# Kernel optimization log

Hardware: AMD Instinct MI355X
Metric: run time of the kernel (lower is better)

## Reference

```python
import jax, jax.numpy as jnp
import numpy as np

ALPHA = 0.2      # LeakyReLU negative slope
NEG = -9e15      # mask fill value from pyGAT dense layer
N, F, H = 4096, 512, 8
NH = F // H      # per-head hidden = 64


def setup_inputs() -> dict:
    key = jax.random.key(0)
    ks = jax.random.split(key, 8)
    x = jax.random.normal(ks[0], (N, F), jnp.float32)
    left = jnp.arange(N, dtype=jnp.int32)  # unused by forward (matches source)
    adj = (jax.random.uniform(ks[1], (N, N)) < 0.01).astype(jnp.float32)
    adj = jnp.minimum(adj + jnp.eye(N, dtype=jnp.float32), 1.0)  # self loops
    Ws = jax.random.normal(ks[2], (H, F, NH), jnp.float32) * (1.0 / np.sqrt(F))
    a1 = jax.random.normal(ks[3], (H, NH), jnp.float32) * 0.1
    a2 = jax.random.normal(ks[4], (H, NH), jnp.float32) * 0.1
    Wo = jax.random.normal(ks[5], (F, F), jnp.float32) * (1.0 / np.sqrt(F))
    ao1 = jax.random.normal(ks[6], (F,), jnp.float32) * 0.1
    ao2 = jax.random.normal(ks[7], (F,), jnp.float32) * 0.1
    return dict(x=x, left=left, adj=adj, Ws=Ws, a1=a1, a2=a2, Wo=Wo, ao1=ao1, ao2=ao2)


def _gat_layer(h, W, a_src, a_dst, adj, concat):
    # h: [N, Fin], W: [Fin, nh]
    Wh = h @ W                                   # [N, nh]
    e = (Wh @ a_src)[:, None] + (Wh @ a_dst)[None, :]   # [N, N]
    e = jnp.where(adj > 0, jax.nn.leaky_relu(e, ALPHA), NEG)
    att = jax.nn.softmax(e, axis=-1)             # row softmax over neighbors
    out = att @ Wh                               # [N, nh]
    return jax.nn.elu(out) if concat else out


def reference(x, left, adj, Ws, a1, a2, Wo, ao1, ao2):
    # multi-head attention (concat=True per head)
    heads = jax.vmap(lambda W, s, d: _gat_layer(x, W, s, d, adj, True))(Ws, a1, a2)  # [H, N, NH]
    hcat = jnp.transpose(heads, (1, 0, 2)).reshape(x.shape[0], H * NH)              # [N, F]
    # output attention layer (concat=False) followed by outer ELU
    out = _gat_layer(hcat, Wo, ao1, ao2, adj, False)
    return jax.nn.elu(out)
```

## Files before the change

kernel.cpp:

```cpp
#include <hip/hip_runtime.h>
#include <hip/hip_bf16.h>
#include <math.h>


#define GN 4096
#define GF 512

typedef __attribute__((ext_vector_type(8))) short bf16x8;
typedef __attribute__((ext_vector_type(4))) float f32x4;
typedef __attribute__((ext_vector_type(2))) _Float16 f16x2;

__device__ inline unsigned short f2bf(float f) {
    unsigned u = __float_as_uint(f);
    return (unsigned short)((u + 0x7fffu + ((u >> 16) & 1u)) >> 16);
}
__device__ inline float bf2f(unsigned short h) {
    return __uint_as_float((unsigned)h << 16);
}
__device__ inline void split2(float v, unsigned short& h, unsigned short& l) {
    h = f2bf(v);
    l = f2bf(v - bf2f(h));
}
__device__ inline void gl16(const void* g, void* l) {
    __builtin_amdgcn_global_load_lds((const __attribute__((address_space(1))) unsigned int*)g,
                                     (__attribute__((address_space(3))) unsigned int*)l, 16, 0, 0);
}

__global__ __launch_bounds__(256) void prep(
        const float* __restrict__ Ws, const float* __restrict__ Wo,
        const float* __restrict__ x,
        unsigned short* __restrict__ wshi, unsigned short* __restrict__ wslo,
        unsigned short* __restrict__ wohi, unsigned short* __restrict__ wolo,
        unsigned short* __restrict__ xhi, unsigned short* __restrict__ xlo) {
    __shared__ float T[64][65];
    int b = blockIdx.x;
    const int t = threadIdx.x;
    if (b < 64) {
        const int h = b >> 3, f0 = (b & 7) * 64;
        #pragma unroll
        for (int i = 0; i < 16; ++i) {
            int idx = i * 256 + t;
            int fr = idx >> 6, k = idx & 63;
            T[fr][k] = Ws[h * 32768 + (f0 + fr) * 64 + k];
        }
        __syncthreads();
        #pragma unroll
        for (int i = 0; i < 16; ++i) {
            int idx = i * 256 + t;
            int k = idx >> 6, fr = idx & 63;
            unsigned short hh, ll;
            split2(T[fr][k], hh, ll);
            size_t dst = (size_t)(h * 64 + k) * 512 + f0 + fr;
            wshi[dst] = hh; wslo[dst] = ll;
        }
        return;
    }
    b -= 64;
    if (b < 64) {
        const int c0 = (b >> 3) * 64, f0 = (b & 7) * 64;
        #pragma unroll
        for (int i = 0; i < 16; ++i) {
            int idx = i * 256 + t;
            int fr = idx >> 6, k = idx & 63;
            T[fr][k] = Wo[(size_t)(f0 + fr) * 512 + c0 + k];
        }
        __syncthreads();
        #pragma unroll
        for (int i = 0; i < 16; ++i) {
            int idx = i * 256 + t;
            int k = idx >> 6, fr = idx & 63;
            unsigned short hh, ll;
            split2(T[fr][k], hh, ll);
            size_t dst = (size_t)(c0 + k) * 512 + f0 + fr;
            wohi[dst] = hh; wolo[dst] = ll;
        }
        return;
    }
    b -= 64;
    {
        int i = b * 256 + t;
        float4 v = ((const float4*)x)[i];
        ushort4 h, l;
        split2(v.x, h.x, l.x); split2(v.y, h.y, l.y);
        split2(v.z, h.z, l.z); split2(v.w, h.w, l.w);
        ((ushort4*)xhi)[i] = h;
        ((ushort4*)xlo)[i] = l;
    }
}

__global__ __launch_bounds__(256) void gemm_3t(
        const unsigned short* __restrict__ Ahi, const unsigned short* __restrict__ Alo,
        const unsigned short* __restrict__ Bhi, const unsigned short* __restrict__ Blo,
        const float* __restrict__ a1v, const float* __restrict__ a2v,
        _Float16* __restrict__ C, float* __restrict__ sdst, float* __restrict__ ddst,
        int M, int K, int Nc) {
    __shared__ char lds[65536];
    const int t = threadIdx.x, lane = t & 63, wid = t >> 6;
    const int blk = blockIdx.x;
    const int bmI = (blk & 7) | ((blk >> 6) << 3);
    const int bnI = (blk >> 3) & 7;
    const int bm0 = bmI * 64, bn0 = bnI * 64;
    const int r0 = t >> 3;
    const int sc8 = (((t & 7) ^ ((t >> 3) & 7)) << 3);
    const size_t aoff = (size_t)(bm0 + r0) * K + sc8;
    const size_t boff = (size_t)(bn0 + r0) * K + sc8;
    const size_t half = (size_t)32 * K;

    auto stage = [&](char* dst, int k0) {
        gl16(Ahi + aoff + k0,        dst + 0 * 4096 + t * 16);
        gl16(Ahi + aoff + half + k0, dst + 1 * 4096 + t * 16);
        gl16(Alo + aoff + k0,        dst + 2 * 4096 + t * 16);
        gl16(Alo + aoff + half + k0, dst + 3 * 4096 + t * 16);
        gl16(Bhi + boff + k0,        dst + 4 * 4096 + t * 16);
        gl16(Bhi + boff + half + k0, dst + 5 * 4096 + t * 16);
        gl16(Blo + boff + k0,        dst + 6 * 4096 + t * 16);
        gl16(Blo + boff + half + k0, dst + 7 * 4096 + t * 16);
    };

    f32x4 acc00 = {0,0,0,0}, acc01 = {0,0,0,0}, acc10 = {0,0,0,0}, acc11 = {0,0,0,0};
    const int mq = (wid >> 1) * 32, nq = (wid & 1) * 32;
    const int rl = lane & 15, hl = lane >> 4;
    const int swz = rl & 7;

    auto compute = [&](const char* Lb) {
        const char* Ah_ = Lb;
        const char* Al_ = Lb + 8192;
        const char* Bh_ = Lb + 16384;
        const char* Bl_ = Lb + 24576;
        #pragma unroll
        for (int s = 0; s < 2; ++s) {
            const int ch = ((s * 4 + hl) ^ swz) * 16;
            const int ra0 = (mq + rl) * 128, ra1 = ra0 + 16 * 128;
            const int rb0 = (nq + rl) * 128, rb1 = rb0 + 16 * 128;
            bf16x8 A0h = *(const bf16x8*)(Ah_ + ra0 + ch);
            bf16x8 A1h = *(const bf16x8*)(Ah_ + ra1 + ch);
            bf16x8 A0l = *(const bf16x8*)(Al_ + ra0 + ch);
            bf16x8 A1l = *(const bf16x8*)(Al_ + ra1 + ch);
            bf16x8 B0h = *(const bf16x8*)(Bh_ + rb0 + ch);
            bf16x8 B1h = *(const bf16x8*)(Bh_ + rb1 + ch);
            bf16x8 B0l = *(const bf16x8*)(Bl_ + rb0 + ch);
            bf16x8 B1l = *(const bf16x8*)(Bl_ + rb1 + ch);
            acc00 = __builtin_amdgcn_mfma_f32_16x16x32_bf16(A0h, B0h, acc00, 0, 0, 0);
            acc01 = __builtin_amdgcn_mfma_f32_16x16x32_bf16(A0h, B1h, acc01, 0, 0, 0);
            acc10 = __builtin_amdgcn_mfma_f32_16x16x32_bf16(A1h, B0h, acc10, 0, 0, 0);
            acc11 = __builtin_amdgcn_mfma_f32_16x16x32_bf16(A1h, B1h, acc11, 0, 0, 0);
            acc00 = __builtin_amdgcn_mfma_f32_16x16x32_bf16(A0h, B0l, acc00, 0, 0, 0);
            acc01 = __builtin_amdgcn_mfma_f32_16x16x32_bf16(A0h, B1l, acc01, 0, 0, 0);
            acc10 = __builtin_amdgcn_mfma_f32_16x16x32_bf16(A1h, B0l, acc10, 0, 0, 0);
            acc11 = __builtin_amdgcn_mfma_f32_16x16x32_bf16(A1h, B1l, acc11, 0, 0, 0);
            acc00 = __builtin_amdgcn_mfma_f32_16x16x32_bf16(A0l, B0h, acc00, 0, 0, 0);
            acc01 = __builtin_amdgcn_mfma_f32_16x16x32_bf16(A0l, B1h, acc01, 0, 0, 0);
            acc10 = __builtin_amdgcn_mfma_f32_16x16x32_bf16(A1l, B0h, acc10, 0, 0, 0);
            acc11 = __builtin_amdgcn_mfma_f32_16x16x32_bf16(A1l, B1h, acc11, 0, 0, 0);
        }
    };

    stage(lds, 0);
    __syncthreads();
    const int NT = K / 64;
    for (int st = 0; st < NT; ++st) {
        char* cur = lds + (st & 1) * 32768;
        if (st + 1 < NT) stage(lds + ((st + 1) & 1) * 32768, (st + 1) * 64);
        compute(cur);
        __syncthreads();
    }

    const int orow = hl * 4;
    #pragma unroll
    for (int j = 0; j < 4; ++j) {
        C[(size_t)(bm0 + mq + orow + j) * Nc + bn0 + nq + rl]           = (_Float16)acc00[j];
        C[(size_t)(bm0 + mq + orow + j) * Nc + bn0 + nq + 16 + rl]      = (_Float16)acc01[j];
        C[(size_t)(bm0 + mq + 16 + orow + j) * Nc + bn0 + nq + rl]      = (_Float16)acc10[j];
        C[(size_t)(bm0 + mq + 16 + orow + j) * Nc + bn0 + nq + 16 + rl] = (_Float16)acc11[j];
    }

    const int C0 = bn0 + nq + rl, C1 = C0 + 16;
    const float a1c0 = a1v[C0], a1c1 = a1v[C1];
    const float a2c0 = a2v[C0], a2c1 = a2v[C1];
    float ps0[4], ps1[4], pd0[4], pd1[4];
    #pragma unroll
    for (int j = 0; j < 4; ++j) {
        ps0[j] = acc00[j] * a1c0 + acc01[j] * a1c1;
        ps1[j] = acc10[j] * a1c0 + acc11[j] * a1c1;
        pd0[j] = acc00[j] * a2c0 + acc01[j] * a2c1;
        pd1[j] = acc10[j] * a2c0 + acc11[j] * a2c1;
    }
    #pragma unroll
    for (int off = 1; off < 16; off <<= 1) {
        #pragma unroll
        for (int j = 0; j < 4; ++j) {
            ps0[j] += __shfl_xor(ps0[j], off);
            ps1[j] += __shfl_xor(ps1[j], off);
            pd0[j] += __shfl_xor(pd0[j], off);
            pd1[j] += __shfl_xor(pd1[j], off);
        }
    }
    float* eps = (float*)lds;
    if ((wid & 1) == 0 && rl == 0) {
        #pragma unroll
        for (int j = 0; j < 4; ++j) {
            eps[mq + orow + j]           = ps0[j];
            eps[mq + 16 + orow + j]      = ps1[j];
            eps[64 + mq + orow + j]      = pd0[j];
            eps[64 + mq + 16 + orow + j] = pd1[j];
        }
    }
    __syncthreads();
    if ((wid & 1) == 1 && rl == 0) {
        #pragma unroll
        for (int j = 0; j < 4; ++j) {
            const int t0 = mq + orow + j, t1 = t0 + 16;
            sdst[(size_t)(bm0 + t0) * 8 + bnI] = ps0[j] + eps[t0];
            sdst[(size_t)(bm0 + t1) * 8 + bnI] = ps1[j] + eps[t1];
            ddst[(size_t)(bm0 + t0) * 8 + bnI] = pd0[j] + eps[64 + t0];
            ddst[(size_t)(bm0 + t1) * 8 + bnI] = pd1[j] + eps[64 + t1];
        }
    }
}

#define PS 516
__global__ __launch_bounds__(256) void attn8_kernel(
        const float* __restrict__ adj,
        const _Float16* __restrict__ Wh, const float* __restrict__ s_t,
        const float* __restrict__ d_t,
        unsigned short* __restrict__ nbr, int* __restrict__ deg,
        unsigned short* __restrict__ ohi, unsigned short* __restrict__ olo, int N) {
    __shared__ int nb[512];
    __shared__ float p[8 * PS];
    __shared__ float lred[8];
    __shared__ int wtot[4];
    const int t = threadIdx.x, lane = t & 63, wid = t >> 6, row = blockIdx.x;

    const float4* arow = (const float4*)(adj + (size_t)row * N);
    unsigned m16 = 0;
    #pragma unroll
    for (int q = 0; q < 4; ++q) {
        float4 v = arow[q * 256 + t];
        if (v.x > 0.f) m16 |= 1u << (q * 4 + 0);
        if (v.y > 0.f) m16 |= 1u << (q * 4 + 1);
        if (v.z > 0.f) m16 |= 1u << (q * 4 + 2);
        if (v.w > 0.f) m16 |= 1u << (q * 4 + 3);
    }
    const int cnt = __popc(m16);
    int inc = cnt;
    #pragma unroll
    for (int off = 1; off < 64; off <<= 1) {
        int nv = __shfl_up(inc, off);
        if (lane >= off) inc += nv;
    }
    if (lane == 63) wtot[wid] = inc;
    __syncthreads();
    int wb = 0;
    #pragma unroll
    for (int w = 0; w < 4; ++w) wb += (w < wid) ? wtot[w] : 0;
    const int M = wtot[0] + wtot[1] + wtot[2] + wtot[3];
    int base = wb + inc - cnt;
    if (t == 0) deg[row] = M;
    {
        unsigned m = m16;
        int k = 0;
        while (m) {
            int b = __ffs(m) - 1;
            m &= m - 1;
            int col = ((b >> 2) << 10) + t * 4 + (b & 3);
            nb[base + k] = col;
            nbr[(size_t)row * 512 + base + k] = (unsigned short)col;
            ++k;
        }
    }
    __syncthreads();

    const float4* sp = (const float4*)(s_t + (size_t)row * 8);
    const float4 sA = sp[0], sB = sp[1];
    const float shv[8] = {sA.x, sA.y, sA.z, sA.w, sB.x, sB.y, sB.z, sB.w};
    for (int j = t; j < M; j += 256) {
        const float4* dp = (const float4*)(d_t + (size_t)nb[j] * 8);
        const float4 dA = dp[0], dB = dp[1];
        const float dv[8] = {dA.x, dA.y, dA.z, dA.w, dB.x, dB.y, dB.z, dB.w};
        #pragma unroll
        for (int h = 0; h < 8; ++h) {
            float e = shv[h] + dv[h];
            e = e > 0.f ? e : 0.2f * e;
            p[h * PS + j] = e;
        }
    }
    __syncthreads();
    const int h = t >> 5, sub = t & 31;
    float lm = -INFINITY;
    for (int j = sub; j < M; j += 32) lm = fmaxf(lm, p[h * PS + j]);
    #pragma unroll
    for (int off = 16; off; off >>= 1) lm = fmaxf(lm, __shfl_xor(lm, off));
    float ls = 0.f;
    for (int j = sub; j < M; j += 32) {
        float pe = __expf(p[h * PS + j] - lm);
        p[h * PS + j] = pe;
        ls += pe;
    }
    #pragma unroll
    for (int off = 16; off; off >>= 1) ls += __shfl_xor(ls, off);
    if (sub == 0) lred[h] = ls;
    __syncthreads();
    const int c = 2 * t;
    const int hc = t >> 5;
    const float inv = 1.f / lred[hc];
    const _Float16* base2 = Wh + c;
    float ax = 0.f, ay = 0.f;
    #pragma unroll 4
    for (int j = 0; j < M; ++j) {
        float pw = p[hc * PS + j];
        const f16x2 w = *(const f16x2*)(base2 + (size_t)nb[j] * 512);
        ax += pw * (float)w.x; ay += pw * (float)w.y;
    }
    ax *= inv; ay *= inv;
    ax = ax > 0.f ? ax : __expf(ax) - 1.f;
    ay = ay > 0.f ? ay : __expf(ay) - 1.f;
    unsigned short hx, lx, hy, ly;
    split2(ax, hx, lx); split2(ay, hy, ly);
    ushort2 hv, lv;
    hv.x = hx; hv.y = hy; lv.x = lx; lv.y = ly;
    *(ushort2*)(ohi + (size_t)row * 512 + c) = hv;
    *(ushort2*)(olo + (size_t)row * 512 + c) = lv;
}

__global__ __launch_bounds__(256) void attn1_kernel(
        const _Float16* __restrict__ Wh, const float* __restrict__ s,
        const float* __restrict__ d, const unsigned short* __restrict__ nbr,
        const int* __restrict__ deg, float* __restrict__ out, int N) {
    __shared__ int nb[512];
    __shared__ float p[512];
    __shared__ float lred[1];
    __shared__ float red[4];
    const int t = threadIdx.x, lane = t & 63, row = blockIdx.x;
    const int M = deg[row];
    for (int j = t; j < M; j += 256) nb[j] = nbr[(size_t)row * 512 + j];
    __syncthreads();
    const float4* sp = (const float4*)(s + (size_t)row * 8);
    float4 s0 = sp[0], s1 = sp[1];
    const float sh = ((s0.x + s0.y) + (s0.z + s0.w)) + ((s1.x + s1.y) + (s1.z + s1.w));
    float lm = -INFINITY;
    for (int j = t; j < M; j += 256) {
        const float4* dp = (const float4*)(d + (size_t)nb[j] * 8);
        float4 d0 = dp[0], d1 = dp[1];
        float dv = ((d0.x + d0.y) + (d0.z + d0.w)) + ((d1.x + d1.y) + (d1.z + d1.w));
        float e = sh + dv;
        e = e > 0.f ? e : 0.2f * e;
        p[j] = e;
        lm = fmaxf(lm, e);
    }
    #pragma unroll
    for (int off = 32; off; off >>= 1) lm = fmaxf(lm, __shfl_xor(lm, off));
    if (lane == 0) red[t >> 6] = lm;
    __syncthreads();
    lm = fmaxf(fmaxf(red[0], red[1]), fmaxf(red[2], red[3]));
    float ls = 0.f;
    for (int j = t; j < M; j += 256) {
        float pe = __expf(p[j] - lm);
        p[j] = pe;
        ls += pe;
    }
    #pragma unroll
    for (int off = 32; off; off >>= 1) ls += __shfl_xor(ls, off);
    __syncthreads();
    if (lane == 0) red[t >> 6] = ls;
    __syncthreads();
    ls = red[0] + red[1] + red[2] + red[3];
    if (t == 0) lred[0] = ls;
    __syncthreads();
    const int c = 2 * t;
    const float inv = 1.f / lred[0];
    const _Float16* base = Wh + c;
    float ax = 0.f, ay = 0.f;
    #pragma unroll 4
    for (int j = 0; j < M; ++j) {
        float pw = p[j];
        const f16x2 w = *(const f16x2*)(base + (size_t)nb[j] * 512);
        ax += pw * (float)w.x; ay += pw * (float)w.y;
    }
    ax *= inv; ay *= inv;
    ax = ax > 0.f ? ax : __expf(ax) - 1.f;
    ay = ay > 0.f ? ay : __expf(ay) - 1.f;
    float2 o; o.x = ax; o.y = ay;
    *(float2*)(out + (size_t)row * 512 + c) = o;
}

extern "C" void kernel_launch(void* const* d_in, const int* in_sizes, int n_in,
                              void* d_out, int out_size, void* d_ws, size_t ws_size,
                              hipStream_t stream) {
    const float* x   = (const float*)d_in[0];
    const float* adj = (const float*)d_in[2];
    const float* Ws  = (const float*)d_in[3];
    const float* a1  = (const float*)d_in[4];
    const float* a2  = (const float*)d_in[5];
    const float* Wo  = (const float*)d_in[6];
    const float* ao1 = (const float*)d_in[7];
    const float* ao2 = (const float*)d_in[8];
    float* out = (float*)d_out;
    const int N = GN;

    char* wsb = (char*)d_ws;
    _Float16* Whh  = (_Float16*)(wsb + 0);
    _Float16* Whoh = (_Float16*)(wsb + 4194304);
    float* s_t   = (float*)(wsb + 8388608);
    float* d_t   = (float*)(wsb + 8519680);
    float* spart = (float*)(wsb + 8650752);
    float* dpart = (float*)(wsb + 8781824);
    unsigned short* nbrs = (unsigned short*)(wsb + 8912896);
    int*            deg  = (int*)(wsb + 13107200);
    unsigned short* xhi  = (unsigned short*)(wsb + 13123584);
    unsigned short* xlo  = (unsigned short*)(wsb + 17317888);
    unsigned short* hch  = (unsigned short*)(wsb + 21512192);
    unsigned short* hcl  = (unsigned short*)(wsb + 25706496);
    unsigned short* wshi = (unsigned short*)(wsb + 29900800);
    unsigned short* wslo = (unsigned short*)(wsb + 30425088);
    unsigned short* wohi = (unsigned short*)(wsb + 30949376);
    unsigned short* wolo = (unsigned short*)(wsb + 31473664);

    hipLaunchKernelGGL(prep, dim3(2176), dim3(256), 0, stream,
                       Ws, Wo, x, wshi, wslo, wohi, wolo, xhi, xlo);
    hipLaunchKernelGGL(gemm_3t, dim3(512), dim3(256), 0, stream,
                       xhi, xlo, wshi, wslo, a1, a2, Whh, s_t, d_t, 4096, 512, 512);
    hipLaunchKernelGGL(attn8_kernel, dim3(4096), dim3(256), 0, stream,
                       adj, Whh, s_t, d_t, nbrs, deg, hch, hcl, N);
    hipLaunchKernelGGL(gemm_3t, dim3(512), dim3(256), 0, stream,
                       hch, hcl, wohi, wolo, ao1, ao2, Whoh, spart, dpart, 4096, 512, 512);
    hipLaunchKernelGGL(attn1_kernel, dim3(4096), dim3(256), 0, stream,
                       Whoh, spart, dpart, nbrs, deg, out, N);
}
```

Before: 76.69 us.

## Process two rows per block in attention kernels with 4-wide fp16 gathers

Both attention kernels now handle two rows per 256-thread block, with 128 threads per row, so the grid is halved. Each thread accumulates four output columns using 8-byte f16x4 gathers instead of two columns with 4-byte loads. This cuts launch and per-block overhead and issues fewer, wider gather loads. Neighbor capacity per row drops from 512 to 256 slots, which is safe only while row degree stays under 256, as it does for this roughly 1%-dense adjacency.

```diff
diff --git a/kernel.cpp b/kernel.cpp
--- a/kernel.cpp
+++ b/kernel.cpp
@@ -5,10 +5,13 @@
 
 #define GN 4096
 #define GF 512
+#define CAP2 256
+#define PS2 260
 
 typedef __attribute__((ext_vector_type(8))) short bf16x8;
 typedef __attribute__((ext_vector_type(4))) float f32x4;
 typedef __attribute__((ext_vector_type(2))) _Float16 f16x2;
+typedef __attribute__((ext_vector_type(4))) _Float16 f16x4;
 
 __device__ inline unsigned short f2bf(float f) {
     unsigned u = __float_as_uint(f);
@@ -218,52 +221,50 @@
     }
 }
 
-#define PS 516
 __global__ __launch_bounds__(256) void attn8_kernel(
         const float* __restrict__ adj,
         const _Float16* __restrict__ Wh, const float* __restrict__ s_t,
         const float* __restrict__ d_t,
         unsigned short* __restrict__ nbr, int* __restrict__ deg,
         unsigned short* __restrict__ ohi, unsigned short* __restrict__ olo, int N) {
-    __shared__ int nb[512];
-    __shared__ float p[8 * PS];
-    __shared__ float lred[8];
+    __shared__ int nb[2][CAP2];
+    __shared__ float p[2][8 * PS2];
+    __shared__ float lred[2][8];
     __shared__ int wtot[4];
-    const int t = threadIdx.x, lane = t & 63, wid = t >> 6, row = blockIdx.x;
+    const int t = threadIdx.x, lane = t & 63, wv = t >> 6;
+    const int rsel = t >> 7, tid = t & 127;
+    const int row = blockIdx.x * 2 + rsel;
 
     const float4* arow = (const float4*)(adj + (size_t)row * N);
-    unsigned m16 = 0;
-    #pragma unroll
-    for (int q = 0; q < 4; ++q) {
-        float4 v = arow[q * 256 + t];
-        if (v.x > 0.f) m16 |= 1u << (q * 4 + 0);
-        if (v.y > 0.f) m16 |= 1u << (q * 4 + 1);
-        if (v.z > 0.f) m16 |= 1u << (q * 4 + 2);
-        if (v.w > 0.f) m16 |= 1u << (q * 4 + 3);
-    }
-    const int cnt = __popc(m16);
+    unsigned m32 = 0;
+    #pragma unroll
+    for (int q = 0; q < 8; ++q) {
+        float4 v = arow[q * 128 + tid];
+        if (v.x > 0.f) m32 |= 1u << (q * 4 + 0);
+        if (v.y > 0.f) m32 |= 1u << (q * 4 + 1);
+        if (v.z > 0.f) m32 |= 1u << (q * 4 + 2);
+        if (v.w > 0.f) m32 |= 1u << (q * 4 + 3);
+    }
+    const int cnt = __popc(m32);
     int inc = cnt;
     #pragma unroll
     for (int off = 1; off < 64; off <<= 1) {
         int nv = __shfl_up(inc, off);
         if (lane >= off) inc += nv;
     }
-    if (lane == 63) wtot[wid] = inc;
-    __syncthreads();
-    int wb = 0;
-    #pragma unroll
-    for (int w = 0; w < 4; ++w) wb += (w < wid) ? wtot[w] : 0;
-    const int M = wtot[0] + wtot[1] + wtot[2] + wtot[3];
-    int base = wb + inc - cnt;
-    if (t == 0) deg[row] = M;
+    if (lane == 63) wtot[wv] = inc;
+    __syncthreads();
+    const int base = inc - cnt + ((wv & 1) ? wtot[rsel * 2] : 0);
+    const int M = wtot[rsel * 2] + wtot[rsel * 2 + 1];
+    if (tid == 0) deg[row] = M;
     {
-        unsigned m = m16;
+        unsigned m = m32;
         int k = 0;
         while (m) {
             int b = __ffs(m) - 1;
             m &= m - 1;
-            int col = ((b >> 2) << 10) + t * 4 + (b & 3);
-            nb[base + k] = col;
+            int col = ((b >> 2) << 9) + tid * 4 + (b & 3);
+            nb[rsel][base + k] = col;
             nbr[(size_t)row * 512 + base + k] = (unsigned short)col;
             ++k;
         }
@@ -273,114 +274,120 @@
     const float4* sp = (const float4*)(s_t + (size_t)row * 8);
     const float4 sA = sp[0], sB = sp[1];
     const float shv[8] = {sA.x, sA.y, sA.z, sA.w, sB.x, sB.y, sB.z, sB.w};
-    for (int j = t; j < M; j += 256) {
-        const float4* dp = (const float4*)(d_t + (size_t)nb[j] * 8);
+    for (int j = tid; j < M; j += 128) {
+        const float4* dp = (const float4*)(d_t + (size_t)nb[rsel][j] * 8);
         const float4 dA = dp[0], dB = dp[1];
         const float dv[8] = {dA.x, dA.y, dA.z, dA.w, dB.x, dB.y, dB.z, dB.w};
         #pragma unroll
         for (int h = 0; h < 8; ++h) {
             float e = shv[h] + dv[h];
             e = e > 0.f ? e : 0.2f * e;
-            p[h * PS + j] = e;
-        }
-    }
-    __syncthreads();
-    const int h = t >> 5, sub = t & 31;
+            p[rsel][h * PS2 + j] = e;
+        }
+    }
+    __syncthreads();
+    const int h = tid >> 4, sub = tid & 15;
     float lm = -INFINITY;
-    for (int j = sub; j < M; j += 32) lm = fmaxf(lm, p[h * PS + j]);
-    #pragma unroll
-    for (int off = 16; off; off >>= 1) lm = fmaxf(lm, __shfl_xor(lm, off));
+    for (int j = sub; j < M; j += 16) lm = fmaxf(lm, p[rsel][h * PS2 + j]);
+    #pragma unroll
+    for (int off = 8; off; off >>= 1) lm = fmaxf(lm, __shfl_xor(lm, off));
     float ls = 0.f;
-    for (int j = sub; j < M; j += 32) {
-        float pe = __expf(p[h * PS + j] - lm);
-        p[h * PS + j] = pe;
+    for (int j = sub; j < M; j += 16) {
+        float pe = __expf(p[rsel][h * PS2 + j] - lm);
+        p[rsel][h * PS2 + j] = pe;
         ls += pe;
     }
     #pragma unroll
-    for (int off = 16; off; off >>= 1) ls += __shfl_xor(ls, off);
-    if (sub == 0) lred[h] = ls;
-    __syncthreads();
-    const int c = 2 * t;
-    const int hc = t >> 5;
-    const float inv = 1.f / lred[hc];
-    const _Float16* base2 = Wh + c;
-    float ax = 0.f, ay = 0.f;
+    for (int off = 8; off; off >>= 1) ls += __shfl_xor(ls, off);
+    if (sub == 0) lred[rsel][h] = ls;
+    __syncthreads();
+    const int c = tid * 4;
+    const int hc = tid >> 4;
+    const float inv = 1.f / lred[rsel][hc];
+    const _Float16* bp = Wh + c;
+    float a0 = 0.f, a1 = 0.f, a2 = 0.f, a3 = 0.f;
     #pragma unroll 4
     for (int j = 0; j < M; ++j) {
-        float pw = p[hc * PS + j];
-        const f16x2 w = *(const f16x2*)(base2 + (size_t)nb[j] * 512);
-        ax += pw * (float)w.x; ay += pw * (float)w.y;
-    }
-    ax *= inv; ay *= inv;
-    ax = ax > 0.f ? ax : __expf(ax) - 1.f;
-    ay = ay > 0.f ? ay : __expf(ay) - 1.f;
-    unsigned short hx, lx, hy, ly;
-    split2(ax, hx, lx); split2(ay, hy, ly);
-    ushort2 hv, lv;
-    hv.x = hx; hv.y = hy; lv.x = lx; lv.y = ly;
-    *(ushort2*)(ohi + (size_t)row * 512 + c) = hv;
-    *(ushort2*)(olo + (size_t)row * 512 + c) = lv;
+        float pw = p[rsel][hc * PS2 + j];
+        const f16x4 w = *(const f16x4*)(bp + (size_t)nb[rsel][j] * 512);
+        a0 += pw * (float)w[0]; a1 += pw * (float)w[1];
+        a2 += pw * (float)w[2]; a3 += pw * (float)w[3];
+    }
+    a0 *= inv; a1 *= inv; a2 *= inv; a3 *= inv;
+    a0 = a0 > 0.f ? a0 : __expf(a0) - 1.f;
+    a1 = a1 > 0.f ? a1 : __expf(a1) - 1.f;
+    a2 = a2 > 0.f ? a2 : __expf(a2) - 1.f;
+    a3 = a3 > 0.f ? a3 : __expf(a3) - 1.f;
+    ushort4 hv, lv;
+    split2(a0, hv.x, lv.x); split2(a1, hv.y, lv.y);
+    split2(a2, hv.z, lv.z); split2(a3, hv.w, lv.w);
+    *(ushort4*)(ohi + (size_t)row * 512 + c) = hv;
+    *(ushort4*)(olo + (size_t)row * 512 + c) = lv;
 }
 
 __global__ __launch_bounds__(256) void attn1_kernel(
         const _Float16* __restrict__ Wh, const float* __restrict__ s,
         const float* __restrict__ d, const unsigned short* __restrict__ nbr,
         const int* __restrict__ deg, float* __restrict__ out, int N) {
-    __shared__ int nb[512];
-    __shared__ float p[512];
-    __shared__ float lred[1];
-    __shared__ float red[4];
-    const int t = threadIdx.x, lane = t & 63, row = blockIdx.x;
+    __shared__ int nb[2][CAP2];
+    __shared__ float p[2][CAP2];
+    __shared__ float redm[4], reds[4];
+    __shared__ float lred[2];
+    const int t = threadIdx.x, lane = t & 63, wv = t >> 6;
+    const int rsel = t >> 7, tid = t & 127;
+    const int row = blockIdx.x * 2 + rsel;
     const int M = deg[row];
-    for (int j = t; j < M; j += 256) nb[j] = nbr[(size_t)row * 512 + j];
+    for (int j = tid; j < M; j += 128)
+        nb[rsel][j] = nbr[(size_t)row * 512 + j];
     __syncthreads();
     const float4* sp = (const float4*)(s + (size_t)row * 8);
     float4 s0 = sp[0], s1 = sp[1];
     const float sh = ((s0.x + s0.y) + (s0.z + s0.w)) + ((s1.x + s1.y) + (s1.z + s1.w));
     float lm = -INFINITY;
-    for (int j = t; j < M; j += 256) {
-        const float4* dp = (const float4*)(d + (size_t)nb[j] * 8);
+    for (int j = tid; j < M; j += 128) {
+        const float4* dp = (const float4*)(d + (size_t)nb[rsel][j] * 8);
         float4 d0 = dp[0], d1 = dp[1];
         float dv = ((d0.x + d0.y) + (d0.z + d0.w)) + ((d1.x + d1.y) + (d1.z + d1.w));
         float e = sh + dv;
         e = e > 0.f ? e : 0.2f * e;
-        p[j] = e;
+        p[rsel][j] = e;
         lm = fmaxf(lm, e);
     }
     #pragma unroll
     for (int off = 32; off; off >>= 1) lm = fmaxf(lm, __shfl_xor(lm, off));
-    if (lane == 0) red[t >> 6] = lm;
-    __syncthreads();
-    lm = fmaxf(fmaxf(red[0], red[1]), fmaxf(red[2], red[3]));
+    if (lane == 0) redm[wv] = lm;
+    __syncthreads();
+    lm = fmaxf(redm[rsel * 2], redm[rsel * 2 + 1]);
     float ls = 0.f;
-    for (int j = t; j < M; j += 256) {
-        float pe = __expf(p[j] - lm);
-        p[j] = pe;
+    for (int j = tid; j < M; j += 128) {
+        float pe = __expf(p[rsel][j] - lm);
+        p[rsel][j] = pe;
         ls += pe;
     }
     #pragma unroll
     for (int off = 32; off; off >>= 1) ls += __shfl_xor(ls, off);
-    __syncthreads();
-    if (lane == 0) red[t >> 6] = ls;
-    __syncthreads();
-    ls = red[0] + red[1] + red[2] + red[3];
-    if (t == 0) lred[0] = ls;
-    __syncthreads();
-    const int c = 2 * t;
-    const float inv = 1.f / lred[0];
-    const _Float16* base = Wh + c;
-    float ax = 0.f, ay = 0.f;
+    if (lane == 0) reds[wv] = ls;
+    __syncthreads();
+    if (tid == 0) lred[rsel] = reds[rsel * 2] + reds[rsel * 2 + 1];
+    __syncthreads();
+    const int c = tid * 4;
+    const float inv = 1.f / lred[rsel];
+    const _Float16* bp = Wh + c;
+    float a0 = 0.f, a1 = 0.f, a2 = 0.f, a3 = 0.f;
     #pragma unroll 4
     for (int j = 0; j < M; ++j) {
-        float pw = p[j];
-        const f16x2 w = *(const f16x2*)(base + (size_t)nb[j] * 512);
-        ax += pw * (float)w.x; ay += pw * (float)w.y;
-    }
-    ax *= inv; ay *= inv;
-    ax = ax > 0.f ? ax : __expf(ax) - 1.f;
-    ay = ay > 0.f ? ay : __expf(ay) - 1.f;
-    float2 o; o.x = ax; o.y = ay;
-    *(float2*)(out + (size_t)row * 512 + c) = o;
+        float pw = p[rsel][j];
+        const f16x4 w = *(const f16x4*)(bp + (size_t)nb[rsel][j] * 512);
+        a0 += pw * (float)w[0]; a1 += pw * (float)w[1];
+        a2 += pw * (float)w[2]; a3 += pw * (float)w[3];
+    }
+    a0 *= inv; a1 *= inv; a2 *= inv; a3 *= inv;
+    a0 = a0 > 0.f ? a0 : __expf(a0) - 1.f;
+    a1 = a1 > 0.f ? a1 : __expf(a1) - 1.f;
+    a2 = a2 > 0.f ? a2 : __expf(a2) - 1.f;
+    a3 = a3 > 0.f ? a3 : __expf(a3) - 1.f;
+    float4 o; o.x = a0; o.y = a1; o.z = a2; o.w = a3;
+    *(float4*)(out + (size_t)row * 512 + c) = o;
 }
 
 extern "C" void kernel_launch(void* const* d_in, const int* in_sizes, int n_in,
@@ -419,10 +426,10 @@
                        Ws, Wo, x, wshi, wslo, wohi, wolo, xhi, xlo);
     hipLaunchKernelGGL(gemm_3t, dim3(512), dim3(256), 0, stream,
                        xhi, xlo, wshi, wslo, a1, a2, Whh, s_t, d_t, 4096, 512, 512);
-    hipLaunchKernelGGL(attn8_kernel, dim3(4096), dim3(256), 0, stream,
+    hipLaunchKernelGGL(attn8_kernel, dim3(2048), dim3(256), 0, stream,
                        adj, Whh, s_t, d_t, nbrs, deg, hch, hcl, N);
     hipLaunchKernelGGL(gemm_3t, dim3(512), dim3(256), 0, stream,
                        hch, hcl, wohi, wolo, ao1, ao2, Whoh, spart, dpart, 4096, 512, 512);
-    hipLaunchKernelGGL(attn1_kernel, dim3(4096), dim3(256), 0, stream,
+    hipLaunchKernelGGL(attn1_kernel, dim3(2048), dim3(256), 0, stream,
                        Whoh, spart, dpart, nbrs, deg, out, N);
 }
```

Result: faster. 74.06 us (-3.4%).
